# Optimization experiments

Hardware: AMD Instinct MI355X
Metric: run time of the kernel (lower is better)

## Reference

```python
import jax, jax.numpy as jnp
import numpy as np
import math

B, S, D_IN, D_Q = 4, 2048, 512, 512

def setup_inputs() -> dict:
    key = jax.random.key(0)
    ks = jax.random.split(key, 7)
    s_in = 1.0 / math.sqrt(D_IN)
    x = jax.random.normal(ks[0], (B, S, D_IN), dtype=jnp.float32)
    # nn.Linear-style params: W [out,in], b [out]; uniform(-1/sqrt(in), 1/sqrt(in))
    Wq = jax.random.uniform(ks[1], (D_Q, D_IN), jnp.float32, -s_in, s_in)
    bq = jax.random.uniform(ks[2], (D_Q,), jnp.float32, -s_in, s_in)
    Wk = jax.random.uniform(ks[3], (D_Q, D_IN), jnp.float32, -s_in, s_in)
    bk = jax.random.uniform(ks[4], (D_Q,), jnp.float32, -s_in, s_in)
    Wv = jax.random.uniform(ks[5], (D_Q, D_IN), jnp.float32, -s_in, s_in)
    bv = jax.random.uniform(ks[6], (D_Q,), jnp.float32, -s_in, s_in)
    return {"x": x, "Wq": Wq, "bq": bq, "Wk": Wk, "bk": bk, "Wv": Wv, "bv": bv}

def reference(x, Wq, bq, Wk, bk, Wv, bv):
    # Q/K/V projections: [B,S,D_IN] @ W^T + b -> [B,S,D_Q]
    Q = jnp.einsum('bsi,qi->bsq', x, Wq) + bq
    K = jnp.einsum('bsi,qi->bsq', x, Wk) + bk
    V = jnp.einsum('bsi,qi->bsq', x, Wv) + bv
    scale = 1.0 / math.sqrt(D_Q)
    scores = jnp.einsum('bsq,btq->bst', Q, K) * scale  # [B,S,S]
    attention = jax.nn.softmax(scores, axis=-1)        # 'atten_prob'
    weighted = jnp.einsum('bst,btq->bsq', attention, V)  # 'atten_score'
    return (attention, weighted)
```

## Files before the change

### kernel.cpp

```cpp
#include <hip/hip_runtime.h>
#include <hip/hip_bf16.h>

typedef unsigned short u16;
typedef short bf16x8 __attribute__((ext_vector_type(8)));
typedef float f32x4 __attribute__((ext_vector_type(4)));

#define S_LEN 2048
#define DQ 512
#define NBATCH 4

__device__ __forceinline__ u16 f2bf(float f) {
    __hip_bfloat16 h = __float2bfloat16(f);
    return *reinterpret_cast<u16*>(&h);
}
__device__ __forceinline__ float bf2f(u16 u) {
    unsigned v = ((unsigned)u) << 16;
    union { unsigned u; float f; } c; c.u = v; return c.f;
}

__device__ __forceinline__ void async16(const u16* g, u16* l) {
    __builtin_amdgcn_global_load_lds(
        (__attribute__((address_space(1))) void*)g,
        (__attribute__((address_space(3))) void*)l, 16, 0, 0);
}

__device__ __forceinline__ int xcd_swz(int bid, int chunk) {
    return (bid & 7) * chunk + (bid >> 3);
}

__global__ __launch_bounds__(256) void k_cvt_all(const float* __restrict__ x,
                                                 const float* __restrict__ wq,
                                                 const float* __restrict__ wk,
                                                 const float* __restrict__ wv,
                                                 u16* __restrict__ xb, u16* __restrict__ wb,
                                                 float* __restrict__ sums) {
    int bid = blockIdx.x;
    if (bid >= 4864) {
        int i = (bid - 4864) * 256 + threadIdx.x;
        *(f32x4*)(sums + (size_t)i * 4) = (f32x4)0.0f;
        return;
    }
    const float* src;
    u16* dst;
    int i;
    if (bid < 4096)      { src = x;  dst = xb;          i = bid * 256 + threadIdx.x; }
    else if (bid < 4352) { src = wq; dst = wb;          i = (bid - 4096) * 256 + threadIdx.x; }
    else if (bid < 4608) { src = wk; dst = wb + 262144; i = (bid - 4352) * 256 + threadIdx.x; }
    else                 { src = wv; dst = wb + 524288; i = (bid - 4608) * 256 + threadIdx.x; }
    f32x4 v = *(const f32x4*)(src + (size_t)i * 4);
    ushort4 o;
    o.x = f2bf(v.x); o.y = f2bf(v.y); o.z = f2bf(v.z); o.w = f2bf(v.w);
    *(ushort4*)(dst + (size_t)i * 4) = o;
}

__device__ __forceinline__ void stage_unit(const u16* __restrict__ G, u16* buf,
                                           int kcol, int h, int tid) {
#pragma unroll
    for (int q = 0; q < 2; ++q) {
        int c   = q * 512 + tid;
        int r   = c >> 3;
        int p   = c & 7;
        int lch = p ^ (r & 7);
        async16(G + (size_t)(h * 128 + r) * DQ + kcol + lch * 8,
                buf + h * 8192 + c * 8);
    }
}

__device__ __forceinline__ void gemm256(const u16* __restrict__ A, const u16* __restrict__ B,
                                        u16* ldsA, u16* ldsB, f32x4 acc[8][4], int tid) {
    const int lane = tid & 63;
    const int w    = tid >> 6;
    const int wr   = w >> 2;
    const int wc   = w & 3;
    const int l16  = lane & 15;
    const int quad = lane >> 4;
    const int p0   = quad ^ (l16 & 7);
    const int a0   = (wr * 128 + l16) * 64 + p0 * 8;
    const int a1   = (wr * 128 + l16) * 64 + (p0 ^ 4) * 8;
    const int b0   = (wc * 64 + l16) * 64 + p0 * 8;
    const int b1   = (wc * 64 + l16) * 64 + (p0 ^ 4) * 8;

    stage_unit(A, ldsA, 0, 0, tid);
    stage_unit(A, ldsA, 0, 1, tid);
    stage_unit(B, ldsB, 0, 0, tid);
    stage_unit(B, ldsB, 0, 1, tid);
    __syncthreads();

    for (int kt = 0; kt < 8; ++kt) {
        const u16* rdA = ldsA + (kt & 1) * 16384;
        const u16* rdB = ldsB + (kt & 1) * 16384;
        u16* wrA = ldsA + ((kt + 1) & 1) * 16384;
        u16* wrB = ldsB + ((kt + 1) & 1) * 16384;
        const int  kc = (kt + 1) * 64;
        const bool pf = kt < 7;
        bf16x8 a[4][2], bbf[2][2];

        if (pf) { stage_unit(A, wrA, kc, 0, tid); stage_unit(A, wrA, kc, 1, tid); }
#pragma unroll
        for (int i = 0; i < 4; ++i) {
            a[i][0] = *(const bf16x8*)(rdA + a0 + i * 1024);
            a[i][1] = *(const bf16x8*)(rdA + a1 + i * 1024);
        }
#pragma unroll
        for (int j = 0; j < 2; ++j) {
            bbf[j][0] = *(const bf16x8*)(rdB + b0 + j * 1024);
            bbf[j][1] = *(const bf16x8*)(rdB + b1 + j * 1024);
        }
        __builtin_amdgcn_s_setprio(1);
#pragma unroll
        for (int i = 0; i < 4; ++i)
#pragma unroll
            for (int j = 0; j < 2; ++j) {
                acc[i][j] = __builtin_amdgcn_mfma_f32_16x16x32_bf16(a[i][0], bbf[j][0], acc[i][j], 0, 0, 0);
                acc[i][j] = __builtin_amdgcn_mfma_f32_16x16x32_bf16(a[i][1], bbf[j][1], acc[i][j], 0, 0, 0);
            }
        __builtin_amdgcn_s_setprio(0);

        if (pf) { stage_unit(B, wrB, kc, 0, tid); stage_unit(B, wrB, kc, 1, tid); }
#pragma unroll
        for (int j = 0; j < 2; ++j) {
            bbf[j][0] = *(const bf16x8*)(rdB + b0 + (2 + j) * 1024);
            bbf[j][1] = *(const bf16x8*)(rdB + b1 + (2 + j) * 1024);
        }
        __builtin_amdgcn_s_setprio(1);
#pragma unroll
        for (int i = 0; i < 4; ++i)
#pragma unroll
            for (int j = 0; j < 2; ++j) {
                acc[i][2 + j] = __builtin_amdgcn_mfma_f32_16x16x32_bf16(a[i][0], bbf[j][0], acc[i][2 + j], 0, 0, 0);
                acc[i][2 + j] = __builtin_amdgcn_mfma_f32_16x16x32_bf16(a[i][1], bbf[j][1], acc[i][2 + j], 0, 0, 0);
            }
        __builtin_amdgcn_s_setprio(0);

#pragma unroll
        for (int i = 0; i < 4; ++i) {
            a[i][0] = *(const bf16x8*)(rdA + a0 + (4 + i) * 1024);
            a[i][1] = *(const bf16x8*)(rdA + a1 + (4 + i) * 1024);
        }
        __builtin_amdgcn_s_setprio(1);
#pragma unroll
        for (int i = 0; i < 4; ++i)
#pragma unroll
            for (int j = 0; j < 2; ++j) {
                acc[4 + i][2 + j] = __builtin_amdgcn_mfma_f32_16x16x32_bf16(a[i][0], bbf[j][0], acc[4 + i][2 + j], 0, 0, 0);
                acc[4 + i][2 + j] = __builtin_amdgcn_mfma_f32_16x16x32_bf16(a[i][1], bbf[j][1], acc[4 + i][2 + j], 0, 0, 0);
            }
        __builtin_amdgcn_s_setprio(0);

#pragma unroll
        for (int j = 0; j < 2; ++j) {
            bbf[j][0] = *(const bf16x8*)(rdB + b0 + j * 1024);
            bbf[j][1] = *(const bf16x8*)(rdB + b1 + j * 1024);
        }
        __builtin_amdgcn_s_setprio(1);
#pragma unroll
        for (int i = 0; i < 4; ++i)
#pragma unroll
            for (int j = 0; j < 2; ++j) {
                acc[4 + i][j] = __builtin_amdgcn_mfma_f32_16x16x32_bf16(a[i][0], bbf[j][0], acc[4 + i][j], 0, 0, 0);
                acc[4 + i][j] = __builtin_amdgcn_mfma_f32_16x16x32_bf16(a[i][1], bbf[j][1], acc[4 + i][j], 0, 0, 0);
            }
        __builtin_amdgcn_s_setprio(0);

        __syncthreads();
    }
}

__global__ __launch_bounds__(512, 2) void k_proj(const u16* __restrict__ xb, const u16* __restrict__ Wb,
                                                 const float* __restrict__ bq, const float* __restrict__ bk,
                                                 const float* __restrict__ bv, u16* __restrict__ out,
                                                 u16* __restrict__ VT) {
    __shared__ __align__(16) u16 lds[65536];
    const int l  = xcd_swz(blockIdx.x, 24);
    const int bx = l & 1;
    const int by = (l >> 1) & 31;
    const int z  = l >> 6;
    const int m0 = by * 256, n0 = bx * 256;
    const u16* A = xb + (size_t)m0 * DQ;
    const u16* B = Wb + (size_t)z * DQ * DQ + (size_t)n0 * DQ;
    const float* bias = (z == 0) ? bq : (z == 1) ? bk : bv;

    f32x4 acc[8][4];
#pragma unroll
    for (int i = 0; i < 8; ++i)
#pragma unroll
        for (int j = 0; j < 4; ++j) acc[i][j] = (f32x4)0.0f;

    const int tid = threadIdx.x;
    gemm256(A, B, lds, lds + 32768, acc, tid);

    const int lane = tid & 63, w = tid >> 6;
    const int wr = w >> 2, wc = w & 3;
    const int l16 = lane & 15, quad = lane >> 4;

    if (z < 2) {
        u16* outz = out + (size_t)z * 8192 * DQ;
#pragma unroll
        for (int j = 0; j < 4; ++j) {
            int gn = n0 + wc * 64 + j * 16 + l16;
            float bv_ = bias[gn];
#pragma unroll
            for (int i = 0; i < 8; ++i)
#pragma unroll
                for (int r = 0; r < 4; ++r) {
                    int gm = m0 + wr * 128 + i * 16 + quad * 4 + r;
                    outz[(size_t)gm * DQ + gn] = f2bf(acc[i][j][r] + bv_);
                }
        }
    } else {
        const int bb_ = m0 >> 11;
        u16* VTb_ = VT + (size_t)bb_ * DQ * S_LEN;
#pragma unroll
        for (int j = 0; j < 4; ++j) {
            int gn = n0 + wc * 64 + j * 16 + l16;
            float bv_ = bias[gn];
#pragma unroll
            for (int i = 0; i < 8; ++i) {
                int t0 = (m0 & 2047) + wr * 128 + i * 16 + quad * 4;
                ushort4 o;
                o.x = f2bf(acc[i][j][0] + bv_);
                o.y = f2bf(acc[i][j][1] + bv_);
                o.z = f2bf(acc[i][j][2] + bv_);
                o.w = f2bf(acc[i][j][3] + bv_);
                *(ushort4*)(VTb_ + (size_t)gn * S_LEN + t0) = o;
            }
        }
    }
}

__global__ __launch_bounds__(512, 2) void k_scores(const u16* __restrict__ Qb, const u16* __restrict__ Kb,
                                                   u16* __restrict__ Pb, float* __restrict__ sums) {
    __shared__ __align__(16) u16 lds[65536];
    const int l  = xcd_swz(blockIdx.x, 32);
    const int bx = l & 7;
    const int by = (l >> 3) & 7;
    const int b  = l >> 6;
    const int m0 = by * 256, n0 = bx * 256;
    const u16* A = Qb + ((size_t)b * S_LEN + m0) * DQ;
    const u16* B = Kb + ((size_t)b * S_LEN + n0) * DQ;

    f32x4 acc[8][4];
#pragma unroll
    for (int i = 0; i < 8; ++i)
#pragma unroll
        for (int j = 0; j < 4; ++j) acc[i][j] = (f32x4)0.0f;

    const int tid = threadIdx.x;
    gemm256(A, B, lds, lds + 32768, acc, tid);

    const float scale = 0.044194173824159216f;
    const int lane = tid & 63, w = tid >> 6;
    const int wr = w >> 2, wc = w & 3;
    const int l16 = lane & 15, quad = lane >> 4;
    u16* prow = Pb + (size_t)(b * S_LEN + m0) * S_LEN;

    float psum[8][4];
#pragma unroll
    for (int i = 0; i < 8; ++i)
#pragma unroll
        for (int r = 0; r < 4; ++r) psum[i][r] = 0.0f;

#pragma unroll
    for (int i = 0; i < 8; ++i)
#pragma unroll
        for (int j = 0; j < 4; ++j)
#pragma unroll
            for (int r = 0; r < 4; ++r) {
                int gm = wr * 128 + i * 16 + quad * 4 + r;
                int gn = n0 + wc * 64 + j * 16 + l16;
                float e = __expf(acc[i][j][r] * scale);
                u16 pbv = f2bf(e);
                prow[(size_t)gm * S_LEN + gn] = pbv;
                psum[i][r] += bf2f(pbv);
            }

    float* sums_row = sums + b * S_LEN + m0 + wr * 128;
#pragma unroll
    for (int i = 0; i < 8; ++i)
#pragma unroll
        for (int r = 0; r < 4; ++r) {
            float v = psum[i][r];
            v += __shfl_xor(v, 1);
            v += __shfl_xor(v, 2);
            v += __shfl_xor(v, 4);
            v += __shfl_xor(v, 8);
            if (l16 == 0) atomicAdd(&sums_row[i * 16 + quad * 4 + r], v);
        }
}

__device__ __forceinline__ void stage_pv(const u16* __restrict__ G, u16* buf,
                                         int kcol, int h, int tid) {
    int c   = tid;
    int r   = c >> 3;
    int p   = c & 7;
    int lch = p ^ (r & 7);
    async16(G + (size_t)(h * 64 + r) * S_LEN + kcol + lch * 8,
            buf + h * 4096 + c * 8);
}

__global__ __launch_bounds__(512, 2) void k_pv(const u16* __restrict__ Pb, const u16* __restrict__ VT,
                                               const float* __restrict__ sums,
                                               float* __restrict__ probs,
                                               float* __restrict__ wout) {
    __shared__ __align__(16) u16 lds[49152];
    u16* ldsA = lds;
    u16* ldsB = lds + 24576;
    const int l  = xcd_swz(blockIdx.x, 32);
    const int bx = l & 3;
    const int by = (l >> 2) & 15;
    const int b  = l >> 6;
    const int m0 = by * 128, n0 = bx * 128;
    const u16* A = Pb + (size_t)(b * S_LEN + m0) * S_LEN;
    const u16* B = VT + (size_t)b * DQ * S_LEN + (size_t)n0 * S_LEN;

    const int tid  = threadIdx.x;
    const int lane = tid & 63;
    const int w    = tid >> 6;
    const int wr   = w >> 2;
    const int wc   = w & 3;
    const int l16  = lane & 15;
    const int quad = lane >> 4;
    const int p0   = quad ^ (l16 & 7);
    const int a0   = (wr * 64 + l16) * 64 + p0 * 8;
    const int a1   = (wr * 64 + l16) * 64 + (p0 ^ 4) * 8;
    const int b0   = (wc * 32 + l16) * 64 + p0 * 8;
    const int b1   = (wc * 32 + l16) * 64 + (p0 ^ 4) * 8;

    f32x4 acc[4][2];
#pragma unroll
    for (int i = 0; i < 4; ++i)
#pragma unroll
        for (int j = 0; j < 2; ++j) acc[i][j] = (f32x4)0.0f;

    stage_pv(A, ldsA, 0, 0, tid);          stage_pv(A, ldsA, 0, 1, tid);
    stage_pv(B, ldsB, 0, 0, tid);          stage_pv(B, ldsB, 0, 1, tid);
    stage_pv(A, ldsA + 8192, 64, 0, tid);  stage_pv(A, ldsA + 8192, 64, 1, tid);
    stage_pv(B, ldsB + 8192, 64, 0, tid);  stage_pv(B, ldsB + 8192, 64, 1, tid);
    asm volatile("s_waitcnt vmcnt(4)" ::: "memory");
    __builtin_amdgcn_s_barrier();
    __builtin_amdgcn_sched_barrier(0);

    int rb = 0;
    for (int kt = 0; kt < 32; ++kt) {
        const u16* rdA = ldsA + rb * 8192;
        const u16* rdB = ldsB + rb * 8192;
        if (kt < 30) {
            int wbi = rb >= 1 ? rb - 1 : 2;
            u16* wA = ldsA + wbi * 8192;
            u16* wB = ldsB + wbi * 8192;
            const int kc = (kt + 2) * 64;
            stage_pv(A, wA, kc, 0, tid);
            stage_pv(A, wA, kc, 1, tid);
            stage_pv(B, wB, kc, 0, tid);
            stage_pv(B, wB, kc, 1, tid);
        }

        bf16x8 a[4][2], bbf[2];
#pragma unroll
        for (int i = 0; i < 4; ++i) {
            a[i][0] = *(const bf16x8*)(rdA + a0 + i * 1024);
            a[i][1] = *(const bf16x8*)(rdA + a1 + i * 1024);
        }
        bbf[0] = *(const bf16x8*)(rdB + b0);
        bbf[1] = *(const bf16x8*)(rdB + b1);
        __builtin_amdgcn_s_setprio(1);
#pragma unroll
        for (int i = 0; i < 4; ++i) {
            acc[i][0] = __builtin_amdgcn_mfma_f32_16x16x32_bf16(a[i][0], bbf[0], acc[i][0], 0, 0, 0);
            acc[i][0] = __builtin_amdgcn_mfma_f32_16x16x32_bf16(a[i][1], bbf[1], acc[i][0], 0, 0, 0);
        }
        __builtin_amdgcn_s_setprio(0);

        bbf[0] = *(const bf16x8*)(rdB + b0 + 1024);
        bbf[1] = *(const bf16x8*)(rdB + b1 + 1024);
        __builtin_amdgcn_s_setprio(1);
#pragma unroll
        for (int i = 0; i < 4; ++i) {
            acc[i][1] = __builtin_amdgcn_mfma_f32_16x16x32_bf16(a[i][0], bbf[0], acc[i][1], 0, 0, 0);
            acc[i][1] = __builtin_amdgcn_mfma_f32_16x16x32_bf16(a[i][1], bbf[1], acc[i][1], 0, 0, 0);
        }
        __builtin_amdgcn_s_setprio(0);

        if (kt < 31) {
            if (kt < 30) asm volatile("s_waitcnt vmcnt(4)" ::: "memory");
            else         asm volatile("s_waitcnt vmcnt(0)" ::: "memory");
            __builtin_amdgcn_s_barrier();
            __builtin_amdgcn_sched_barrier(0);
        }
        rb = (rb == 2) ? 0 : rb + 1;
    }

    float* ldsInv = (float*)lds;
    if (tid < 128) ldsInv[tid] = 1.0f / sums[b * S_LEN + m0 + tid];
    __syncthreads();

    float* outb = wout + (size_t)b * S_LEN * DQ;
#pragma unroll
    for (int i = 0; i < 4; ++i) {
#pragma unroll
        for (int r = 0; r < 4; ++r) {
            int lm = wr * 64 + i * 16 + quad * 4 + r;
            float inv = ldsInv[lm];
#pragma unroll
            for (int j = 0; j < 2; ++j) {
                int gn = n0 + wc * 32 + j * 16 + l16;
                outb[(size_t)(m0 + lm) * DQ + gn] = acc[i][j][r] * inv;
            }
        }
    }

    const u16* Psl = Pb + (size_t)(b * S_LEN + m0) * S_LEN + bx * 512;
    float* Pro = probs + ((size_t)b * S_LEN + m0) * S_LEN + bx * 512;
#pragma unroll
    for (int it = 0; it < 16; ++it) {
        int idx = it * 512 + tid;
        int r  = idx >> 6;
        int cc = (idx & 63) << 3;
        float inv = ldsInv[r];
        bf16x8 vv = *(const bf16x8*)(Psl + (size_t)r * S_LEN + cc);
        f32x4 o0, o1;
        o0.x = bf2f((u16)vv[0]) * inv;
        o0.y = bf2f((u16)vv[1]) * inv;
        o0.z = bf2f((u16)vv[2]) * inv;
        o0.w = bf2f((u16)vv[3]) * inv;
        o1.x = bf2f((u16)vv[4]) * inv;
        o1.y = bf2f((u16)vv[5]) * inv;
        o1.z = bf2f((u16)vv[6]) * inv;
        o1.w = bf2f((u16)vv[7]) * inv;
        float* dst = Pro + (size_t)r * S_LEN + cc;
        *(f32x4*)(dst) = o0;
        *(f32x4*)(dst + 4) = o1;
    }
}

extern "C" void kernel_launch(void* const* d_in, const int* in_sizes, int n_in,
                              void* d_out, int out_size, void* d_ws, size_t ws_size,
                              hipStream_t stream) {
    const float* x  = (const float*)d_in[0];
    const float* Wq = (const float*)d_in[1];
    const float* bq = (const float*)d_in[2];
    const float* Wk = (const float*)d_in[3];
    const float* bk = (const float*)d_in[4];
    const float* Wv = (const float*)d_in[5];
    const float* bv = (const float*)d_in[6];

    char* ws = (char*)d_ws;
    u16* xb  = (u16*)(ws);
    u16* Wb  = (u16*)(ws + 8388608);
    u16* Qb  = (u16*)(ws + 9961472);
    u16* Kb  = (u16*)(ws + 18350080);
    u16* VTb = (u16*)(ws + 35127296);
    u16* Pb  = (u16*)(ws + 43515904);
    float* sums = (float*)(ws + 77070336);
    float* probs = (float*)d_out;
    float* wout  = (float*)d_out + 16777216;

    k_cvt_all<<<4872, 256, 0, stream>>>(x, Wq, Wk, Wv, xb, Wb, sums);
    k_proj<<<192, 512, 0, stream>>>(xb, Wb, bq, bk, bv, Qb, VTb);
    k_scores<<<256, 512, 0, stream>>>(Qb, Kb, Pb, sums);
    k_pv<<<256, 512, 0, stream>>>(Pb, VTb, sums, probs, wout);
}
```

Baseline: 182.2 us.

## Interleave probability normalization stores into the PV MFMA main loop

Moves the epilogue that reads bf16 unnormalized probabilities, scales them by the inverse row sums and writes fp32 probs into the k-loop, handling one chunk every other iteration. The inverse sums are loaded before the loop into a dedicated LDS region, and the vmcnt waits are raised to account for the extra load and stores in flight. The aim is to hide the large fp32 probs write traffic behind the MFMA work instead of running it as a serialized tail. In exchange it adds memory traffic and VGPR pressure inside the pipelined loop and relies on hand-tuned waitcnt counts.

After: 177.9 us. 1.02x faster.

```diff
diff --git a/kernel.cpp b/kernel.cpp
--- a/kernel.cpp
+++ b/kernel.cpp
@@ -302,9 +302,10 @@
                                                const float* __restrict__ sums,
                                                float* __restrict__ probs,
                                                float* __restrict__ wout) {
-    __shared__ __align__(16) u16 lds[49152];
+    __shared__ __align__(16) u16 lds[49408];
     u16* ldsA = lds;
     u16* ldsB = lds + 24576;
+    float* ldsInv = (float*)(lds + 49152);
     const int l  = xcd_swz(blockIdx.x, 32);
     const int bx = l & 3;
     const int by = (l >> 2) & 15;
@@ -312,6 +313,8 @@
     const int m0 = by * 128, n0 = bx * 128;
     const u16* A = Pb + (size_t)(b * S_LEN + m0) * S_LEN;
     const u16* B = VT + (size_t)b * DQ * S_LEN + (size_t)n0 * S_LEN;
+    const u16* Psl = Pb + (size_t)(b * S_LEN + m0) * S_LEN + bx * 512;
+    float* Pro = probs + ((size_t)b * S_LEN + m0) * S_LEN + bx * 512;
 
     const int tid  = threadIdx.x;
     const int lane = tid & 63;
@@ -332,11 +335,14 @@
 #pragma unroll
         for (int j = 0; j < 2; ++j) acc[i][j] = (f32x4)0.0f;
 
+    float sv = 1.0f;
+    if (tid < 128) sv = sums[b * S_LEN + m0 + tid];
     stage_pv(A, ldsA, 0, 0, tid);          stage_pv(A, ldsA, 0, 1, tid);
     stage_pv(B, ldsB, 0, 0, tid);          stage_pv(B, ldsB, 0, 1, tid);
     stage_pv(A, ldsA + 8192, 64, 0, tid);  stage_pv(A, ldsA + 8192, 64, 1, tid);
     stage_pv(B, ldsB + 8192, 64, 0, tid);  stage_pv(B, ldsB + 8192, 64, 1, tid);
-    asm volatile("s_waitcnt vmcnt(4)" ::: "memory");
+    if (tid < 128) ldsInv[tid] = 1.0f / sv;
+    asm volatile("s_waitcnt vmcnt(4) lgkmcnt(0)" ::: "memory");
     __builtin_amdgcn_s_barrier();
     __builtin_amdgcn_sched_barrier(0);
 
@@ -344,6 +350,20 @@
     for (int kt = 0; kt < 32; ++kt) {
         const u16* rdA = ldsA + rb * 8192;
         const u16* rdB = ldsB + rb * 8192;
+
+        const bool do_probs = (kt & 1) == 0;
+        bf16x8 pvv;
+        float pinv = 0.0f;
+        float* pdst = nullptr;
+        if (do_probs) {
+            int idx = (kt >> 1) * 512 + tid;
+            int r  = idx >> 6;
+            int cc = (idx & 63) << 3;
+            pvv  = *(const bf16x8*)(Psl + (size_t)r * S_LEN + cc);
+            pinv = ldsInv[r];
+            pdst = Pro + (size_t)r * S_LEN + cc;
+        }
+
         if (kt < 30) {
             int wbi = rb >= 1 ? rb - 1 : 2;
             u16* wA = ldsA + wbi * 8192;
@@ -381,18 +401,28 @@
         }
         __builtin_amdgcn_s_setprio(0);
 
+        if (do_probs) {
+            f32x4 o0, o1;
+            o0.x = bf2f((u16)pvv[0]) * pinv;
+            o0.y = bf2f((u16)pvv[1]) * pinv;
+            o0.z = bf2f((u16)pvv[2]) * pinv;
+            o0.w = bf2f((u16)pvv[3]) * pinv;
+            o1.x = bf2f((u16)pvv[4]) * pinv;
+            o1.y = bf2f((u16)pvv[5]) * pinv;
+            o1.z = bf2f((u16)pvv[6]) * pinv;
+            o1.w = bf2f((u16)pvv[7]) * pinv;
+            *(f32x4*)(pdst) = o0;
+            *(f32x4*)(pdst + 4) = o1;
+        }
+
         if (kt < 31) {
-            if (kt < 30) asm volatile("s_waitcnt vmcnt(4)" ::: "memory");
-            else         asm volatile("s_waitcnt vmcnt(0)" ::: "memory");
+            if (kt < 30) asm volatile("s_waitcnt vmcnt(6)" ::: "memory");
+            else         asm volatile("s_waitcnt vmcnt(2)" ::: "memory");
             __builtin_amdgcn_s_barrier();
             __builtin_amdgcn_sched_barrier(0);
         }
         rb = (rb == 2) ? 0 : rb + 1;
     }
-
-    float* ldsInv = (float*)lds;
-    if (tid < 128) ldsInv[tid] = 1.0f / sums[b * S_LEN + m0 + tid];
-    __syncthreads();
 
     float* outb = wout + (size_t)b * S_LEN * DQ;
 #pragma unroll
@@ -407,29 +437,6 @@
                 outb[(size_t)(m0 + lm) * DQ + gn] = acc[i][j][r] * inv;
             }
         }
-    }
-
-    const u16* Psl = Pb + (size_t)(b * S_LEN + m0) * S_LEN + bx * 512;
-    float* Pro = probs + ((size_t)b * S_LEN + m0) * S_LEN + bx * 512;
-#pragma unroll
-    for (int it = 0; it < 16; ++it) {
-        int idx = it * 512 + tid;
-        int r  = idx >> 6;
-        int cc = (idx & 63) << 3;
-        float inv = ldsInv[r];
-        bf16x8 vv = *(const bf16x8*)(Psl + (size_t)r * S_LEN + cc);
-        f32x4 o0, o1;
-        o0.x = bf2f((u16)vv[0]) * inv;
-        o0.y = bf2f((u16)vv[1]) * inv;
-        o0.z = bf2f((u16)vv[2]) * inv;
-        o0.w = bf2f((u16)vv[3]) * inv;
-        o1.x = bf2f((u16)vv[4]) * inv;
-        o1.y = bf2f((u16)vv[5]) * inv;
-        o1.z = bf2f((u16)vv[6]) * inv;
-        o1.w = bf2f((u16)vv[7]) * inv;
-        float* dst = Pro + (size_t)r * S_LEN + cc;
-        *(f32x4*)(dst) = o0;
-        *(f32x4*)(dst + 4) = o1;
     }
 }
 
```
